# Kernel optimization log

Hardware: AMD Instinct MI355X
Metric: run time of the kernel (lower is better)

## Reference

```python
import jax, jax.numpy as jnp
import numpy as np

N, NFEAT, NHID, NCLASS, NLAYERS = 8192, 512, 128, 40, 3
NEG = -9e15

def _sparse_adj(key, n, density=0.002):
    u = jax.random.uniform(key, (n, n), dtype=jnp.float32)
    return jnp.where(u < density, u / density, 0.0)

def setup_inputs() -> dict:
    key = jax.random.key(0)
    ks = jax.random.split(key, 12)
    return {
        "x": jax.random.normal(ks[0], (N, NFEAT), dtype=jnp.float32),
        "adj1": _sparse_adj(ks[1], N),
        "adj2": _sparse_adj(ks[2], N),
        "adj_att": _sparse_adj(ks[3], N),
        "fc1_w": jax.random.normal(ks[4], (NLAYERS, NHID, NFEAT), dtype=jnp.float32) * (1.0 / np.sqrt(NFEAT)),
        "fc1_b": jnp.zeros((NLAYERS, NHID), jnp.float32),
        "Q_w": jax.random.normal(ks[5], (NLAYERS - 1, NHID, NHID), dtype=jnp.float32) * (1.0 / np.sqrt(NHID)),
        "Q_b": jnp.zeros((NLAYERS - 1, NHID), jnp.float32),
        "K_w": jax.random.normal(ks[6], (NLAYERS - 1, NHID, NHID), dtype=jnp.float32) * (1.0 / np.sqrt(NHID)),
        "K_b": jnp.zeros((NLAYERS - 1, NHID), jnp.float32),
        "hop_select": jnp.ones((NLAYERS,), jnp.float32),
        "w": jnp.ones((NLAYERS - 1, 2), jnp.float32),
        "clf_w": jax.random.normal(ks[7], (NCLASS, NHID * NLAYERS), dtype=jnp.float32) * (1.0 / np.sqrt(NHID * NLAYERS)),
        "clf_b": jnp.zeros((NCLASS,), jnp.float32),
    }

def _l2_normalize(x, eps=1e-12):
    # F.normalize(x, p=2, dim=1)
    n = jnp.sqrt(jnp.sum(x * x, axis=1, keepdims=True))
    return x / jnp.maximum(n, eps)

def reference(x, adj1, adj2, adj_att, fc1_w, fc1_b, Q_w, Q_b, K_w, K_b,
              hop_select, w, clf_w, clf_b):
    adj_list = [None, adj1, adj2]
    mask = jax.nn.softmax(hop_select)  # hop selection weights, shape [nlayers]
    outs = []
    for i in range(NLAYERS):
        tmp = x @ fc1_w[i].T + fc1_b[i]  # [N, nhid]
        if adj_list[i] is not None:
            adj = adj_list[i]
            W_att = jax.nn.softmax(w[i - 1])  # [2]
            tmp_att = adj_att @ tmp           # [N, nhid]
            # GCN1: linear then propagate with adj_att (act='None')
            Q = adj_att @ (tmp_att @ Q_w[i - 1].T + Q_b[i - 1])
            K = adj_att @ (tmp_att @ K_w[i - 1].T + K_b[i - 1])
            scores = Q @ K.T                  # [N, N]
            scores = jnp.where(adj > 0, scores, NEG)
            attention = jax.nn.softmax(scores, axis=-1) * W_att[0] + adj * W_att[1]
            tmp = attention @ tmp             # [N, nhid]
        tmp = _l2_normalize(tmp)
        outs.append(mask[i] * tmp)
    final = jnp.concatenate(outs, axis=1)     # [N, nhid*nlayers]
    out = jax.nn.relu(final) @ clf_w.T + clf_b  # dropout is identity in eval
    return jax.nn.log_softmax(out, axis=1)
```

## Files before the change

### kernel.cpp

```cpp
#include <hip/hip_runtime.h>
#include <hip/hip_bf16.h>

#define NN     8192
#define NF4    2048
#define NFEAT  512
#define NHID   128
#define NCLASS 40
#define NLAY   3
#define CAPA   128
#define FSZ    ((size_t)NN * NHID)

typedef float f32x4 __attribute__((ext_vector_type(4)));

__global__ void k_setup(const float* __restrict__ hop, const float* __restrict__ w,
                        float* __restrict__ mask, float* __restrict__ watt,
                        float* __restrict__ colsum) {
    int t = threadIdx.x;
    colsum[t] = 0.f;
    if (t == 0) {
        float m = fmaxf(fmaxf(hop[0], hop[1]), hop[2]);
        float e0 = expf(hop[0] - m), e1 = expf(hop[1] - m), e2 = expf(hop[2] - m);
        float s = e0 + e1 + e2;
        mask[0] = e0 / s; mask[1] = e1 / s; mask[2] = e2 / s;
        for (int l = 0; l < 2; ++l) {
            float a = w[2 * l], b = w[2 * l + 1];
            float mm = fmaxf(a, b);
            float ea = expf(a - mm), eb = expf(b - mm);
            float ss = ea + eb;
            watt[2 * l] = ea / ss; watt[2 * l + 1] = eb / ss;
        }
    }
}

__global__ __launch_bounds__(256, 4) void k_scan_fc1(
    const float* __restrict__ x, const float* __restrict__ fc1w, const float* __restrict__ fc1b,
    const float* __restrict__ adjA, const float* __restrict__ adj1, const float* __restrict__ adj2,
    float* __restrict__ tmps, float* __restrict__ colsum, float* __restrict__ rowsumA,
    int* __restrict__ cnts, int* __restrict__ colsArr, float* __restrict__ valsArr)
{
    __shared__ float smem[6400];
    __shared__ int s_lcnt;
    __shared__ float s_lsum;
    const int bx = blockIdx.x, plane = blockIdx.y, tid = threadIdx.x;

    if (bx < 128) {
        float* As = smem;
        float* Bs = smem + 2176;
        const int tx = tid & 15, ty = tid >> 4;
        const int bm = bx * 64;
        const int layer = plane;
        const int bn = layer * 128;
        float acc[4][8] = {};

        for (int kt = 0; kt < NFEAT; kt += 32) {
            #pragma unroll
            for (int it = 0; it < 2; ++it) {
                int L = tid + it * 256;
                int r = L >> 3, c4 = (L & 7) * 4;
                f32x4 va = *reinterpret_cast<const f32x4*>(&x[(size_t)(bm + r) * NFEAT + kt + c4]);
                As[(c4 + 0) * 68 + r] = va[0];
                As[(c4 + 1) * 68 + r] = va[1];
                As[(c4 + 2) * 68 + r] = va[2];
                As[(c4 + 3) * 68 + r] = va[3];
            }
            #pragma unroll
            for (int it = 0; it < 4; ++it) {
                int L = tid + it * 256;
                int r = L >> 3, c4 = (L & 7) * 4;
                f32x4 vb = *reinterpret_cast<const f32x4*>(&fc1w[(size_t)(bn + r) * NFEAT + kt + c4]);
                Bs[(c4 + 0) * 132 + r] = vb[0];
                Bs[(c4 + 1) * 132 + r] = vb[1];
                Bs[(c4 + 2) * 132 + r] = vb[2];
                Bs[(c4 + 3) * 132 + r] = vb[3];
            }
            __syncthreads();
            #pragma unroll
            for (int kk = 0; kk < 32; ++kk) {
                f32x4 ra  = *reinterpret_cast<const f32x4*>(&As[kk * 68 + ty * 4]);
                f32x4 rb0 = *reinterpret_cast<const f32x4*>(&Bs[kk * 132 + tx * 4]);
                f32x4 rb1 = *reinterpret_cast<const f32x4*>(&Bs[kk * 132 + tx * 4 + 64]);
                #pragma unroll
                for (int i = 0; i < 4; ++i) {
                    #pragma unroll
                    for (int j = 0; j < 4; ++j) {
                        acc[i][j]     = fmaf(ra[i], rb0[j], acc[i][j]);
                        acc[i][j + 4] = fmaf(ra[i], rb1[j], acc[i][j + 4]);
                    }
                }
            }
            __syncthreads();
        }
        const float* bofs = fc1b + bn;
        #pragma unroll
        for (int i = 0; i < 4; ++i) {
            int m = bm + ty * 4 + i;
            #pragma unroll
            for (int j = 0; j < 8; ++j) {
                int lc = (j < 4) ? (tx * 4 + j) : (64 + tx * 4 + (j - 4));
                tmps[(size_t)layer * FSZ + (size_t)m * NHID + lc] = acc[i][j] + bofs[lc];
            }
        }
        if (layer >= 1) {
            #pragma unroll
            for (int j = 0; j < 8; ++j) {
                int lc = (j < 4) ? (tx * 4 + j) : (64 + tx * 4 + (j - 4));
                float s = 4.f * bofs[lc];
                #pragma unroll
                for (int i = 0; i < 4; ++i) s += acc[i][j];
                smem[ty * 128 + lc] = s;
            }
            __syncthreads();
            if (tid < 128) {
                float s = 0.f;
                #pragma unroll
                for (int g = 0; g < 16; ++g) s += smem[g * 128 + tid];
                atomicAdd(&colsum[(layer - 1) * NHID + tid], s);
            }
        }
    } else {
        const int row = bx - 128, mat = plane;
        const float* adj = (mat == 0) ? adjA : (mat == 1 ? adj1 : adj2);
        if (tid == 0) { s_lcnt = 0; s_lsum = 0.f; }
        __syncthreads();
        const f32x4* arow = reinterpret_cast<const f32x4*>(adj + (size_t)row * NN);
        int* rc = colsArr + (size_t)(mat * NN + row) * CAPA;
        float* rv = valsArr + (size_t)(mat * NN + row) * CAPA;
        float ls = 0.f;
        for (int c4 = tid; c4 < NF4; c4 += 256) {
            f32x4 v = __builtin_nontemporal_load(&arow[c4]);
            #pragma unroll
            for (int k = 0; k < 4; ++k) {
                if (v[k] > 0.f) {
                    int p = atomicAdd(&s_lcnt, 1);
                    if (p < CAPA) { rc[p] = c4 * 4 + k; rv[p] = v[k]; }
                    ls += v[k];
                }
            }
        }
        if (mat == 0 && ls != 0.f) atomicAdd(&s_lsum, ls);
        __syncthreads();
        if (tid == 0) {
            cnts[mat * NN + row] = s_lcnt < CAPA ? s_lcnt : CAPA;
            if (mat == 0) rowsumA[row] = s_lsum;
        }
    }
}

__global__ __launch_bounds__(128) void k_sp_norm(
    const int* __restrict__ cnts, const int* __restrict__ colsArr, const float* __restrict__ valsArr,
    const float* __restrict__ tmps, const float* __restrict__ mask,
    float* __restrict__ tmp_att, float* __restrict__ outsb)
{
    int row = blockIdx.x, role = blockIdx.y, t = threadIdx.x;
    __shared__ int sc[CAPA];
    __shared__ float sv[CAPA];
    __shared__ float wsn[2];
    if (role == 2) {
        float v = tmps[(size_t)row * NHID + t];
        float s = v * v;
        #pragma unroll
        for (int m = 32; m; m >>= 1) s += __shfl_xor(s, m);
        if ((t & 63) == 0) wsn[t >> 6] = s;
        __syncthreads();
        float d = fmaxf(sqrtf(wsn[0] + wsn[1]), 1e-12f);
        outsb[(size_t)row * (NHID * NLAY) + t] = mask[0] * v / d;
    } else {
        const float* X = tmps + (size_t)(role + 1) * FSZ;
        float* Y = tmp_att + (size_t)role * FSZ;
        int n = cnts[row];
        for (int p = t; p < n; p += 128) { sc[p] = colsArr[(size_t)row * CAPA + p]; sv[p] = valsArr[(size_t)row * CAPA + p]; }
        __syncthreads();
        float a0 = 0.f, a1 = 0.f, a2 = 0.f, a3 = 0.f;
        int p = 0;
        for (; p + 4 <= n; p += 4) {
            a0 = fmaf(sv[p],     X[(size_t)sc[p]     * NHID + t], a0);
            a1 = fmaf(sv[p + 1], X[(size_t)sc[p + 1] * NHID + t], a1);
            a2 = fmaf(sv[p + 2], X[(size_t)sc[p + 2] * NHID + t], a2);
            a3 = fmaf(sv[p + 3], X[(size_t)sc[p + 3] * NHID + t], a3);
        }
        for (; p < n; ++p) a0 = fmaf(sv[p], X[(size_t)sc[p] * NHID + t], a0);
        Y[(size_t)row * NHID + t] = (a0 + a1) + (a2 + a3);
    }
}

__global__ __launch_bounds__(256, 2) void k_t2qkm(
    const int* __restrict__ cnts, const int* __restrict__ colsArr, const float* __restrict__ valsArr,
    const float* __restrict__ tmp_att, const float* __restrict__ Qw, const float* __restrict__ Kw,
    const float* __restrict__ Qb, const float* __restrict__ Kb,
    const float* __restrict__ rowsumA, float* __restrict__ QKm)
{
    __shared__ float AsT[128 * 64];
    __shared__ float Bs[128 * 64];
    const int tid = threadIdx.x;
    const int bm = blockIdx.x * 64, Lz = blockIdx.y;
    const float* X = tmp_att + (size_t)Lz * FSZ;

    {
        const int lrow = tid >> 2, coff = (tid & 3) * 32;
        const int row = bm + lrow;
        f32x4 acc[8] = {};
        const int n = cnts[row];
        const int* rc = colsArr + (size_t)row * CAPA;
        const float* rv = valsArr + (size_t)row * CAPA;
        for (int p = 0; p < n; ++p) {
            int c = rc[p];
            float v = rv[p];
            const f32x4* src = reinterpret_cast<const f32x4*>(X + (size_t)c * NHID + coff);
            #pragma unroll
            for (int j = 0; j < 8; ++j) {
                f32x4 s = src[j];
                acc[j][0] = fmaf(v, s[0], acc[j][0]);
                acc[j][1] = fmaf(v, s[1], acc[j][1]);
                acc[j][2] = fmaf(v, s[2], acc[j][2]);
                acc[j][3] = fmaf(v, s[3], acc[j][3]);
            }
        }
        #pragma unroll
        for (int j = 0; j < 8; ++j)
            #pragma unroll
            for (int q = 0; q < 4; ++q)
                AsT[(coff + j * 4 + q) * 64 + lrow] = acc[j][q];
    }
    __syncthreads();

    const int tx = tid & 15, ty = tid >> 4;
    float rs[4];
    #pragma unroll
    for (int i = 0; i < 4; ++i) rs[i] = rowsumA[bm + ty * 4 + i];
    float* C = QKm + (size_t)Lz * NN * 256;

    for (int ch = 0; ch < 4; ++ch) {
        const int bn = ch * 64;
        const float* Bp; const float* bp; int bc;
        if (bn < 128) { Bp = Qw + (size_t)Lz * NHID * NHID; bp = Qb + (size_t)Lz * NHID; bc = bn; }
        else          { Bp = Kw + (size_t)Lz * NHID * NHID; bp = Kb + (size_t)Lz * NHID; bc = bn - 128; }
        {
            int r = tid >> 2, c0 = (tid & 3) * 32;
            #pragma unroll
            for (int j = 0; j < 8; ++j) {
                f32x4 v = *reinterpret_cast<const f32x4*>(&Bp[(size_t)(bc + r) * NHID + c0 + j * 4]);
                #pragma unroll
                for (int q = 0; q < 4; ++q) Bs[(c0 + j * 4 + q) * 64 + r] = v[q];
            }
        }
        __syncthreads();
        float acc[4][4] = {};
        #pragma unroll 8
        for (int kk = 0; kk < 128; ++kk) {
            f32x4 ra = *reinterpret_cast<const f32x4*>(&AsT[kk * 64 + ty * 4]);
            f32x4 rb = *reinterpret_cast<const f32x4*>(&Bs[kk * 64 + tx * 4]);
            #pragma unroll
            for (int i = 0; i < 4; ++i)
                #pragma unroll
                for (int j = 0; j < 4; ++j)
                    acc[i][j] = fmaf(ra[i], rb[j], acc[i][j]);
        }
        #pragma unroll
        for (int i = 0; i < 4; ++i) {
            int m = bm + ty * 4 + i;
            #pragma unroll
            for (int j = 0; j < 4; ++j) {
                int nc = bn + tx * 4 + j;
                C[(size_t)m * 256 + nc] = acc[i][j] + rs[i] * bp[bc + tx * 4 + j];
            }
        }
        __syncthreads();
    }
}

__global__ __launch_bounds__(256) void k_attn(
    const int* __restrict__ cnts, const int* __restrict__ colsArr, const float* __restrict__ valsArr,
    const float* __restrict__ QKm, const float* __restrict__ tmps,
    const float* __restrict__ colsum, const float* __restrict__ watt,
    const float* __restrict__ mask, float* __restrict__ outsb)
{
    int row = blockIdx.x, L = blockIdx.y, t = threadIdx.x;
    const float* QK = QKm + (size_t)L * NN * 256;
    const float* T = tmps + (size_t)(L + 1) * FSZ;
    const int* rc = colsArr + (size_t)((1 + L) * NN + row) * CAPA;
    const float* rv = valsArr + (size_t)((1 + L) * NN + row) * CAPA;
    __shared__ int cols[CAPA];
    __shared__ float avals[CAPA];
    __shared__ float svals[CAPA];
    __shared__ __align__(16) float qrow[NHID];
    __shared__ float psum[2][NHID];
    __shared__ float ws[4];

    int n = cnts[(1 + L) * NN + row];
    for (int p = t; p < n; p += 256) { cols[p] = rc[p]; avals[p] = rv[p]; }
    if (t < 32) *reinterpret_cast<f32x4*>(&qrow[t * 4]) =
        *reinterpret_cast<const f32x4*>(QK + (size_t)row * 256 + t * 4);
    __syncthreads();

    float W0 = watt[L * 2], W1 = watt[L * 2 + 1];
    float acc = 0.f;

    if (n > 0) {
        int g = t >> 5, sl = t & 31;
        f32x4 qv = *reinterpret_cast<const f32x4*>(&qrow[sl * 4]);
        for (int p = g; p < n; p += 8) {
            f32x4 kv = *reinterpret_cast<const f32x4*>(QK + (size_t)cols[p] * 256 + 128 + sl * 4);
            float s = qv[0] * kv[0] + qv[1] * kv[1] + qv[2] * kv[2] + qv[3] * kv[3];
            #pragma unroll
            for (int m = 16; m; m >>= 1) s += __shfl_xor(s, m);
            if (sl == 0) svals[p] = s;
        }
        __syncthreads();
        if (t < 64) {
            float mx = -3.0e38f;
            for (int p = t; p < n; p += 64) mx = fmaxf(mx, svals[p]);
            #pragma unroll
            for (int m = 32; m; m >>= 1) mx = fmaxf(mx, __shfl_xor(mx, m));
            float ss = 0.f;
            for (int p = t; p < n; p += 64) ss += expf(svals[p] - mx);
            #pragma unroll
            for (int m = 32; m; m >>= 1) ss += __shfl_xor(ss, m);
            float inv = 1.0f / ss;
            for (int p = t; p < n; p += 64) avals[p] = expf(svals[p] - mx) * inv * W0 + avals[p] * W1;
        }
        __syncthreads();
        int half = t >> 7, tt = t & 127;
        float pacc = 0.f;
        for (int p = half; p < n; p += 2) pacc = fmaf(avals[p], T[(size_t)cols[p] * NHID + tt], pacc);
        psum[half][tt] = pacc;
        __syncthreads();
        if (t < 128) acc = psum[0][t] + psum[1][t];
    } else {
        if (t < 128) acc = W0 * (1.0f / (float)NN) * colsum[L * NHID + t];
    }

    float s2 = acc * acc;
    #pragma unroll
    for (int m = 32; m; m >>= 1) s2 += __shfl_xor(s2, m);
    if ((t & 63) == 0) ws[t >> 6] = s2;
    __syncthreads();
    if (t < 128) {
        float d = fmaxf(sqrtf(ws[0] + ws[1]), 1e-12f);
        outsb[(size_t)row * (NHID * NLAY) + (size_t)(L + 1) * NHID + t] = mask[L + 1] * acc / d;
    }
}

__global__ __launch_bounds__(64) void k_clf(
    const float* __restrict__ outs, const float* __restrict__ Wc,
    const float* __restrict__ bc, float* __restrict__ out)
{
    __shared__ float fin[NHID * NLAY];
    __shared__ float logits[NCLASS];
    int t = threadIdx.x;
    for (int rr = 0; rr < 2; ++rr) {
        int row = blockIdx.x * 2 + rr;
        for (int k = t; k < NHID * NLAY; k += 64) fin[k] = fmaxf(outs[(size_t)row * (NHID * NLAY) + k], 0.f);
        __syncthreads();
        if (t < NCLASS) {
            float acc = bc[t];
            #pragma unroll 4
            for (int k = 0; k < NHID * NLAY; ++k) acc = fmaf(fin[k], Wc[(size_t)t * (NHID * NLAY) + k], acc);
            logits[t] = acc;
        }
        __syncthreads();
        float x = (t < NCLASS) ? logits[t] : -3.0e38f;
        float mx = x;
        #pragma unroll
        for (int m = 32; m; m >>= 1) mx = fmaxf(mx, __shfl_xor(mx, m));
        float e = (t < NCLASS) ? expf(x - mx) : 0.f;
        float ssum = e;
        #pragma unroll
        for (int m = 32; m; m >>= 1) ssum += __shfl_xor(ssum, m);
        if (t < NCLASS) out[(size_t)row * NCLASS + t] = x - mx - logf(ssum);
        __syncthreads();
    }
}

extern "C" void kernel_launch(void* const* d_in, const int* in_sizes, int n_in,
                              void* d_out, int out_size, void* d_ws, size_t ws_size,
                              hipStream_t stream) {
    const float* x       = (const float*)d_in[0];
    const float* adj1    = (const float*)d_in[1];
    const float* adj2    = (const float*)d_in[2];
    const float* adj_att = (const float*)d_in[3];
    const float* fc1_w   = (const float*)d_in[4];
    const float* fc1_b   = (const float*)d_in[5];
    const float* Q_w     = (const float*)d_in[6];
    const float* Q_b     = (const float*)d_in[7];
    const float* K_w     = (const float*)d_in[8];
    const float* K_b     = (const float*)d_in[9];
    const float* hop     = (const float*)d_in[10];
    const float* w       = (const float*)d_in[11];
    const float* clf_w   = (const float*)d_in[12];
    const float* clf_b   = (const float*)d_in[13];

    float* W = (float*)d_ws;
    float* f_mask   = W;
    float* f_watt   = W + 4;
    float* f_colsum = W + 8;
    float* rowsumA  = W + 264;
    float* tmps     = W + 264 + NN;
    float* outsb    = tmps + 3 * FSZ;
    float* tmp_att  = outsb + 3 * FSZ;
    float* QKm      = tmp_att + 2 * FSZ;
    float* csr_vals = QKm + 4 * FSZ;
    int*   csr_cols = (int*)(csr_vals + 3 * FSZ);
    int*   csr_cnt  = csr_cols + 3 * FSZ;

    size_t need = (size_t)((char*)(csr_cnt + 3 * NN) - (char*)d_ws);
    if (ws_size < need) return;

    k_setup<<<1, 256, 0, stream>>>(hop, w, f_mask, f_watt, f_colsum);

    k_scan_fc1<<<dim3(128 + NN, 3), 256, 0, stream>>>(
        x, fc1_w, fc1_b, adj_att, adj1, adj2,
        tmps, f_colsum, rowsumA, csr_cnt, csr_cols, csr_vals);

    k_sp_norm<<<dim3(NN, 3), 128, 0, stream>>>(
        csr_cnt, csr_cols, csr_vals, tmps, f_mask, tmp_att, outsb);

    k_t2qkm<<<dim3(NN / 64, 2), 256, 0, stream>>>(
        csr_cnt, csr_cols, csr_vals, tmp_att, Q_w, K_w, Q_b, K_b, rowsumA, QKm);

    k_attn<<<dim3(NN, 2), 256, 0, stream>>>(
        csr_cnt, csr_cols, csr_vals, QKm, tmps, f_colsum, f_watt, f_mask, outsb);

    k_clf<<<NN / 2, 64, 0, stream>>>(outsb, clf_w, clf_b, (float*)d_out);
}
```

Measured before the change: 373.3 us.

## Fold setup into scan kernel, move colsum to spmm, fuse layer-0 norm into classifier

Merges the setup work (softmax of hop/w and zeroing colsum) into an extra block of the scan/fc1 kernel, removing one launch. The column-sum reduction moves out of the GEMM epilogue into extra blocks of the sparse-matmul kernel. The layer-0 L2 normalisation moves from a separate role into the classifier kernel, and the classifier now handles two rows per block with one wave each. The adjacency scan issues all eight row loads up front to raise memory-level parallelism. One risk: colsum is zeroed in the same launch as the scan, while the atomics that accumulate into it run in the next kernel, so ordering still depends on stream serialisation.

Result: faster. 356.4 us (-4.5%).

```diff
diff --git a/kernel.cpp b/kernel.cpp
--- a/kernel.cpp
+++ b/kernel.cpp
@@ -12,30 +12,12 @@
 
 typedef float f32x4 __attribute__((ext_vector_type(4)));
 
-__global__ void k_setup(const float* __restrict__ hop, const float* __restrict__ w,
-                        float* __restrict__ mask, float* __restrict__ watt,
-                        float* __restrict__ colsum) {
-    int t = threadIdx.x;
-    colsum[t] = 0.f;
-    if (t == 0) {
-        float m = fmaxf(fmaxf(hop[0], hop[1]), hop[2]);
-        float e0 = expf(hop[0] - m), e1 = expf(hop[1] - m), e2 = expf(hop[2] - m);
-        float s = e0 + e1 + e2;
-        mask[0] = e0 / s; mask[1] = e1 / s; mask[2] = e2 / s;
-        for (int l = 0; l < 2; ++l) {
-            float a = w[2 * l], b = w[2 * l + 1];
-            float mm = fmaxf(a, b);
-            float ea = expf(a - mm), eb = expf(b - mm);
-            float ss = ea + eb;
-            watt[2 * l] = ea / ss; watt[2 * l + 1] = eb / ss;
-        }
-    }
-}
-
 __global__ __launch_bounds__(256, 4) void k_scan_fc1(
     const float* __restrict__ x, const float* __restrict__ fc1w, const float* __restrict__ fc1b,
     const float* __restrict__ adjA, const float* __restrict__ adj1, const float* __restrict__ adj2,
-    float* __restrict__ tmps, float* __restrict__ colsum, float* __restrict__ rowsumA,
+    const float* __restrict__ hop, const float* __restrict__ w,
+    float* __restrict__ tmps, float* __restrict__ f_mask, float* __restrict__ f_watt,
+    float* __restrict__ colsum, float* __restrict__ rowsumA,
     int* __restrict__ cnts, int* __restrict__ colsArr, float* __restrict__ valsArr)
 {
     __shared__ float smem[6400];
@@ -100,24 +82,7 @@
                 tmps[(size_t)layer * FSZ + (size_t)m * NHID + lc] = acc[i][j] + bofs[lc];
             }
         }
-        if (layer >= 1) {
-            #pragma unroll
-            for (int j = 0; j < 8; ++j) {
-                int lc = (j < 4) ? (tx * 4 + j) : (64 + tx * 4 + (j - 4));
-                float s = 4.f * bofs[lc];
-                #pragma unroll
-                for (int i = 0; i < 4; ++i) s += acc[i][j];
-                smem[ty * 128 + lc] = s;
-            }
-            __syncthreads();
-            if (tid < 128) {
-                float s = 0.f;
-                #pragma unroll
-                for (int g = 0; g < 16; ++g) s += smem[g * 128 + tid];
-                atomicAdd(&colsum[(layer - 1) * NHID + tid], s);
-            }
-        }
-    } else {
+    } else if (bx < 128 + NN) {
         const int row = bx - 128, mat = plane;
         const float* adj = (mat == 0) ? adjA : (mat == 1 ? adj1 : adj2);
         if (tid == 0) { s_lcnt = 0; s_lsum = 0.f; }
@@ -125,15 +90,22 @@
         const f32x4* arow = reinterpret_cast<const f32x4*>(adj + (size_t)row * NN);
         int* rc = colsArr + (size_t)(mat * NN + row) * CAPA;
         float* rv = valsArr + (size_t)(mat * NN + row) * CAPA;
+
+        f32x4 v[8];
+        #pragma unroll
+        for (int i = 0; i < 8; ++i)
+            v[i] = __builtin_nontemporal_load(&arow[tid + (i << 8)]);
+
         float ls = 0.f;
-        for (int c4 = tid; c4 < NF4; c4 += 256) {
-            f32x4 v = __builtin_nontemporal_load(&arow[c4]);
+        #pragma unroll
+        for (int i = 0; i < 8; ++i) {
+            const int c4 = tid + (i << 8);
             #pragma unroll
             for (int k = 0; k < 4; ++k) {
-                if (v[k] > 0.f) {
+                if (v[i][k] > 0.f) {
                     int p = atomicAdd(&s_lcnt, 1);
-                    if (p < CAPA) { rc[p] = c4 * 4 + k; rv[p] = v[k]; }
-                    ls += v[k];
+                    if (p < CAPA) { rc[p] = c4 * 4 + k; rv[p] = v[i][k]; }
+                    ls += v[i][k];
                 }
             }
         }
@@ -143,44 +115,55 @@
             cnts[mat * NN + row] = s_lcnt < CAPA ? s_lcnt : CAPA;
             if (mat == 0) rowsumA[row] = s_lsum;
         }
-    }
-}
-
-__global__ __launch_bounds__(128) void k_sp_norm(
+    } else if (plane == 0) {
+        colsum[tid] = 0.f;
+        if (tid == 0) {
+            float m = fmaxf(fmaxf(hop[0], hop[1]), hop[2]);
+            float e0 = expf(hop[0] - m), e1 = expf(hop[1] - m), e2 = expf(hop[2] - m);
+            float s = e0 + e1 + e2;
+            f_mask[0] = e0 / s; f_mask[1] = e1 / s; f_mask[2] = e2 / s;
+            for (int l = 0; l < 2; ++l) {
+                float a = w[2 * l], b = w[2 * l + 1];
+                float mm = fmaxf(a, b);
+                float ea = expf(a - mm), eb = expf(b - mm);
+                float ss = ea + eb;
+                f_watt[2 * l] = ea / ss; f_watt[2 * l + 1] = eb / ss;
+            }
+        }
+    }
+}
+
+__global__ __launch_bounds__(128) void k_spmm_cs(
     const int* __restrict__ cnts, const int* __restrict__ colsArr, const float* __restrict__ valsArr,
-    const float* __restrict__ tmps, const float* __restrict__ mask,
-    float* __restrict__ tmp_att, float* __restrict__ outsb)
+    const float* __restrict__ tmps, float* __restrict__ tmp_att, float* __restrict__ colsum)
 {
-    int row = blockIdx.x, role = blockIdx.y, t = threadIdx.x;
+    int bx = blockIdx.x, L = blockIdx.y, t = threadIdx.x;
+    if (bx >= NN) {
+        int c = bx - NN;
+        const float* X = tmps + (size_t)(L + 1) * FSZ + (size_t)c * 128 * NHID;
+        float a = 0.f;
+        for (int r = 0; r < 128; ++r) a += X[(size_t)r * NHID + t];
+        atomicAdd(&colsum[L * NHID + t], a);
+        return;
+    }
+    int row = bx;
+    const float* X = tmps + (size_t)(L + 1) * FSZ;
+    float* Y = tmp_att + (size_t)L * FSZ;
     __shared__ int sc[CAPA];
     __shared__ float sv[CAPA];
-    __shared__ float wsn[2];
-    if (role == 2) {
-        float v = tmps[(size_t)row * NHID + t];
-        float s = v * v;
-        #pragma unroll
-        for (int m = 32; m; m >>= 1) s += __shfl_xor(s, m);
-        if ((t & 63) == 0) wsn[t >> 6] = s;
-        __syncthreads();
-        float d = fmaxf(sqrtf(wsn[0] + wsn[1]), 1e-12f);
-        outsb[(size_t)row * (NHID * NLAY) + t] = mask[0] * v / d;
-    } else {
-        const float* X = tmps + (size_t)(role + 1) * FSZ;
-        float* Y = tmp_att + (size_t)role * FSZ;
-        int n = cnts[row];
-        for (int p = t; p < n; p += 128) { sc[p] = colsArr[(size_t)row * CAPA + p]; sv[p] = valsArr[(size_t)row * CAPA + p]; }
-        __syncthreads();
-        float a0 = 0.f, a1 = 0.f, a2 = 0.f, a3 = 0.f;
-        int p = 0;
-        for (; p + 4 <= n; p += 4) {
-            a0 = fmaf(sv[p],     X[(size_t)sc[p]     * NHID + t], a0);
-            a1 = fmaf(sv[p + 1], X[(size_t)sc[p + 1] * NHID + t], a1);
-            a2 = fmaf(sv[p + 2], X[(size_t)sc[p + 2] * NHID + t], a2);
-            a3 = fmaf(sv[p + 3], X[(size_t)sc[p + 3] * NHID + t], a3);
-        }
-        for (; p < n; ++p) a0 = fmaf(sv[p], X[(size_t)sc[p] * NHID + t], a0);
-        Y[(size_t)row * NHID + t] = (a0 + a1) + (a2 + a3);
-    }
+    int n = cnts[row];
+    for (int p = t; p < n; p += 128) { sc[p] = colsArr[(size_t)row * CAPA + p]; sv[p] = valsArr[(size_t)row * CAPA + p]; }
+    __syncthreads();
+    float a0 = 0.f, a1 = 0.f, a2 = 0.f, a3 = 0.f;
+    int p = 0;
+    for (; p + 4 <= n; p += 4) {
+        a0 = fmaf(sv[p],     X[(size_t)sc[p]     * NHID + t], a0);
+        a1 = fmaf(sv[p + 1], X[(size_t)sc[p + 1] * NHID + t], a1);
+        a2 = fmaf(sv[p + 2], X[(size_t)sc[p + 2] * NHID + t], a2);
+        a3 = fmaf(sv[p + 3], X[(size_t)sc[p + 3] * NHID + t], a3);
+    }
+    for (; p < n; ++p) a0 = fmaf(sv[p], X[(size_t)sc[p] * NHID + t], a0);
+    Y[(size_t)row * NHID + t] = (a0 + a1) + (a2 + a3);
 }
 
 __global__ __launch_bounds__(256, 2) void k_t2qkm(
@@ -340,35 +323,50 @@
     }
 }
 
-__global__ __launch_bounds__(64) void k_clf(
-    const float* __restrict__ outs, const float* __restrict__ Wc,
-    const float* __restrict__ bc, float* __restrict__ out)
+__global__ __launch_bounds__(128) void k_clf(
+    const float* __restrict__ tmps0, const float* __restrict__ outs,
+    const float* __restrict__ Wc, const float* __restrict__ bc,
+    const float* __restrict__ mask, float* __restrict__ out)
 {
-    __shared__ float fin[NHID * NLAY];
-    __shared__ float logits[NCLASS];
-    int t = threadIdx.x;
-    for (int rr = 0; rr < 2; ++rr) {
-        int row = blockIdx.x * 2 + rr;
-        for (int k = t; k < NHID * NLAY; k += 64) fin[k] = fmaxf(outs[(size_t)row * (NHID * NLAY) + k], 0.f);
-        __syncthreads();
-        if (t < NCLASS) {
-            float acc = bc[t];
-            #pragma unroll 4
-            for (int k = 0; k < NHID * NLAY; ++k) acc = fmaf(fin[k], Wc[(size_t)t * (NHID * NLAY) + k], acc);
-            logits[t] = acc;
-        }
-        __syncthreads();
-        float x = (t < NCLASS) ? logits[t] : -3.0e38f;
-        float mx = x;
-        #pragma unroll
-        for (int m = 32; m; m >>= 1) mx = fmaxf(mx, __shfl_xor(mx, m));
-        float e = (t < NCLASS) ? expf(x - mx) : 0.f;
-        float ssum = e;
-        #pragma unroll
-        for (int m = 32; m; m >>= 1) ssum += __shfl_xor(ssum, m);
-        if (t < NCLASS) out[(size_t)row * NCLASS + t] = x - mx - logf(ssum);
-        __syncthreads();
-    }
+    __shared__ float fin[2][NHID * NLAY];
+    const int t = threadIdx.x, wv = t >> 6, lane = t & 63;
+    const int row = blockIdx.x * 2 + wv;
+
+    float v0 = tmps0[(size_t)row * NHID + lane];
+    float v1 = tmps0[(size_t)row * NHID + 64 + lane];
+    float s = v0 * v0 + v1 * v1;
+    #pragma unroll
+    for (int m = 32; m; m >>= 1) s += __shfl_xor(s, m);
+    float d = fmaxf(sqrtf(s), 1e-12f);
+    float m0 = mask[0];
+    fin[wv][lane]      = fmaxf(m0 * v0 / d, 0.f);
+    fin[wv][64 + lane] = fmaxf(m0 * v1 / d, 0.f);
+    #pragma unroll
+    for (int k = 0; k < 4; ++k)
+        fin[wv][128 + k * 64 + lane] = fmaxf(outs[(size_t)row * (NHID * NLAY) + 128 + k * 64 + lane], 0.f);
+    __syncthreads();
+
+    float logit = -3.0e38f;
+    if (lane < NCLASS) {
+        const float* wrow = Wc + (size_t)lane * (NHID * NLAY);
+        float a0 = 0.f, a1 = 0.f, a2 = 0.f, a3 = 0.f;
+        #pragma unroll 4
+        for (int k = 0; k < NHID * NLAY; k += 4) {
+            a0 = fmaf(fin[wv][k],     wrow[k],     a0);
+            a1 = fmaf(fin[wv][k + 1], wrow[k + 1], a1);
+            a2 = fmaf(fin[wv][k + 2], wrow[k + 2], a2);
+            a3 = fmaf(fin[wv][k + 3], wrow[k + 3], a3);
+        }
+        logit = bc[lane] + (a0 + a1) + (a2 + a3);
+    }
+    float mx = logit;
+    #pragma unroll
+    for (int m = 32; m; m >>= 1) mx = fmaxf(mx, __shfl_xor(mx, m));
+    float e = (lane < NCLASS) ? expf(logit - mx) : 0.f;
+    float ssum = e;
+    #pragma unroll
+    for (int m = 32; m; m >>= 1) ssum += __shfl_xor(ssum, m);
+    if (lane < NCLASS) out[(size_t)row * NCLASS + lane] = logit - mx - logf(ssum);
 }
 
 extern "C" void kernel_launch(void* const* d_in, const int* in_sizes, int n_in,
@@ -405,14 +403,12 @@
     size_t need = (size_t)((char*)(csr_cnt + 3 * NN) - (char*)d_ws);
     if (ws_size < need) return;
 
-    k_setup<<<1, 256, 0, stream>>>(hop, w, f_mask, f_watt, f_colsum);
-
-    k_scan_fc1<<<dim3(128 + NN, 3), 256, 0, stream>>>(
-        x, fc1_w, fc1_b, adj_att, adj1, adj2,
-        tmps, f_colsum, rowsumA, csr_cnt, csr_cols, csr_vals);
-
-    k_sp_norm<<<dim3(NN, 3), 128, 0, stream>>>(
-        csr_cnt, csr_cols, csr_vals, tmps, f_mask, tmp_att, outsb);
+    k_scan_fc1<<<dim3(NN + 129, 3), 256, 0, stream>>>(
+        x, fc1_w, fc1_b, adj_att, adj1, adj2, hop, w,
+        tmps, f_mask, f_watt, f_colsum, rowsumA, csr_cnt, csr_cols, csr_vals);
+
+    k_spmm_cs<<<dim3(NN + 64, 2), 128, 0, stream>>>(
+        csr_cnt, csr_cols, csr_vals, tmps, tmp_att, f_colsum);
 
     k_t2qkm<<<dim3(NN / 64, 2), 256, 0, stream>>>(
         csr_cnt, csr_cols, csr_vals, tmp_att, Q_w, K_w, Q_b, K_b, rowsumA, QKm);
@@ -420,5 +416,5 @@
     k_attn<<<dim3(NN, 2), 256, 0, stream>>>(
         csr_cnt, csr_cols, csr_vals, QKm, tmps, f_colsum, f_watt, f_mask, outsb);
 
-    k_clf<<<NN / 2, 64, 0, stream>>>(outsb, clf_w, clf_b, (float*)d_out);
-}
+    k_clf<<<NN / 2, 128, 0, stream>>>(tmps, outsb, clf_w, clf_b, f_mask, (float*)d_out);
+}
```
